# Performance work log

Measured on AMD Instinct MI355X. Metric: run time of the kernel, lower is better.

The kernel has to match this reference:

```python
import jax, jax.numpy as jnp
import numpy as np

B, S, P = 2, 1024, 1024          # batch, new tokens, start_pos (cached prefix)
E, H, KV, HD = 2048, 32, 8, 64    # embed, heads, kv groups, head_dim
G = H // KV                       # group size = 4
THETA = 500000.0
CTX = P + S                       # cache/context length = 2048


def _rope_tables(start, seqlen):
    inv_freq = 1.0 / (THETA ** (jnp.arange(0, HD, 2, dtype=jnp.float32) / HD))
    pos = jnp.arange(start, start + seqlen, dtype=jnp.float32)
    freqs = jnp.outer(pos, inv_freq)              # [S, HD/2]
    emb = jnp.concatenate([freqs, freqs], axis=-1)  # [S, HD]
    return jnp.cos(emb), jnp.sin(emb)


def setup_inputs() -> dict:
    key = jax.random.key(0)
    ks = jax.random.split(key, 8)
    x = jax.random.normal(ks[0], (B, S, E), dtype=jnp.float32)
    cos1, sin1 = _rope_tables(P, S)
    cos = jnp.broadcast_to(cos1[None], (B, S, HD))
    sin = jnp.broadcast_to(sin1[None], (B, S, HD))
    # causal-with-offset additive mask: query i (global pos P+i) sees key j <= P+i
    qpos = P + jnp.arange(S)[:, None]
    kpos = jnp.arange(CTX)[None, :]
    mask = jnp.where(kpos <= qpos, 0.0, -1e9).astype(jnp.float32)[None, None]  # [1,1,S,CTX]
    cache_k = jax.random.normal(ks[1], (B, KV, CTX, HD), dtype=jnp.float32)
    cache_v = jax.random.normal(ks[2], (B, KV, CTX, HD), dtype=jnp.float32)
    sc = 0.02
    Wq = jax.random.normal(ks[3], (E, E), dtype=jnp.float32) * sc
    Wk = jax.random.normal(ks[4], (KV * HD, E), dtype=jnp.float32) * sc
    Wv = jax.random.normal(ks[5], (KV * HD, E), dtype=jnp.float32) * sc
    Wo = jax.random.normal(ks[6], (E, E), dtype=jnp.float32) * sc
    return {"x": x, "cos": cos, "sin": sin, "mask": mask,
            "cache_k": cache_k, "cache_v": cache_v,
            "Wq": Wq, "Wk": Wk, "Wv": Wv, "Wo": Wo, "start_pos": P}


def _rotate_half(t):
    t1, t2 = t[..., : HD // 2], t[..., HD // 2:]
    return jnp.concatenate([-t2, t1], axis=-1)


def _apply_rope(t, cos, sin):
    # t: [B, nh, S, HD]; cos/sin: [B, S, HD] -> unsqueeze head dim
    c = cos[:, None]
    s = sin[:, None]
    return t * c + _rotate_half(t) * s


def reference(x, cos, sin, mask, cache_k, cache_v, Wq, Wk, Wv, Wo, start_pos):
    b, s, e = x.shape
    q = (x @ Wq.T).reshape(b, s, H, HD).transpose(0, 2, 1, 3)    # [B,H,S,HD]
    k = (x @ Wk.T).reshape(b, s, KV, HD).transpose(0, 2, 1, 3)   # [B,KV,S,HD]
    v = (x @ Wv.T).reshape(b, s, KV, HD).transpose(0, 2, 1, 3)
    q = _apply_rope(q, cos, sin)
    k = _apply_rope(k, cos, sin)
    ck = cache_k.at[:, :, start_pos:start_pos + s].set(k)
    cv = cache_v.at[:, :, start_pos:start_pos + s].set(v)
    keys = ck[:, :, : start_pos + s]      # [B,KV,T,HD]
    vals = cv[:, :, : start_pos + s]
    # GQA without materializing repeated KV: view q as [B,KV,G,S,HD]
    qg = q.reshape(b, KV, G, s, HD)
    scores = jnp.einsum("bkgsh,bkth->bkgst", qg, keys) / jnp.sqrt(jnp.float32(HD))
    scores = scores + mask[:, :, None]    # broadcast mask over group dim
    probs = jax.nn.softmax(scores.astype(jnp.float32), axis=-1).astype(x.dtype)
    out = jnp.einsum("bkgst,bkth->bkgsh", probs, vals)            # [B,KV,G,S,HD]
    out = out.reshape(b, H, s, HD).transpose(0, 2, 1, 3).reshape(b, s, e)
    return out @ Wo.T
```

## Files before the change

### kernel.cpp

```cpp
#include <hip/hip_runtime.h>
#include <cstddef>

#define B   2
#define S   1024
#define PP  1024
#define CTX 2048
#define E   2048
#define H   32
#define KVH 8
#define HD  64
#define GQ  4
#define NQKV 3072

typedef short s4v  __attribute__((ext_vector_type(4)));
typedef short s8v  __attribute__((ext_vector_type(8)));
typedef float f4v  __attribute__((ext_vector_type(4)));

__device__ __forceinline__ short f2bf(float f) {
  union { float f; unsigned u; } v; v.f = f;
  unsigned r = v.u + 0x7fffu + ((v.u >> 16) & 1u);
  return (short)(r >> 16);
}
__device__ __forceinline__ float bf2f(short h) {
  union { unsigned u; float f; } v; v.u = ((unsigned)(unsigned short)h) << 16;
  return v.f;
}

__device__ __forceinline__ void gl_lds16(const void* g, void* l) {
  __builtin_amdgcn_global_load_lds((const __attribute__((address_space(1))) unsigned*)g,
                                   (__attribute__((address_space(3))) unsigned*)l, 16, 0, 0);
}

__global__ __launch_bounds__(256) void prep(const float* __restrict__ x,
                                            const float* __restrict__ Wq,
                                            const float* __restrict__ Wk,
                                            const float* __restrict__ Wv,
                                            short* __restrict__ xb,
                                            short* __restrict__ wqkv) {
  const int blk = blockIdx.x, tid = threadIdx.x;
  const float* s; short* d; int base;
  if (blk < 2048)      { s = x;  d = xb;             base = blk; }
  else if (blk < 4096) { s = Wq; d = wqkv;           base = blk - 2048; }
  else if (blk < 4608) { s = Wk; d = wqkv + 4194304; base = blk - 4096; }
  else                 { s = Wv; d = wqkv + 5242880; base = blk - 4608; }
  int i = (base * 256 + tid) * 8;
  float4 a = *(const float4*)&s[i];
  float4 b = *(const float4*)&s[i + 4];
  s8v o;
  o[0]=f2bf(a.x); o[1]=f2bf(a.y); o[2]=f2bf(a.z); o[3]=f2bf(a.w);
  o[4]=f2bf(b.x); o[5]=f2bf(b.y); o[6]=f2bf(b.z); o[7]=f2bf(b.w);
  *(s8v*)&d[i] = o;
}

__global__ __launch_bounds__(256) void qkv_gemm(const short* __restrict__ A,
                                                const short* __restrict__ Bw,
                                                const float* __restrict__ cosb,
                                                const float* __restrict__ sinb,
                                                const float* __restrict__ Wo,
                                                const float* __restrict__ ck,
                                                const float* __restrict__ cv,
                                                short* __restrict__ qb,
                                                short* __restrict__ keys,
                                                short* __restrict__ vt,
                                                short* __restrict__ wob,
                                                float4* __restrict__ outz) {
  __shared__ short As[2][8192];
  __shared__ short Bs[2][8192];
  const int tid = threadIdx.x;
  const int id  = blockIdx.x;

  if (id >= 384) {
    const int aux = id - 384;
    if (aux < 2048) {
      int i = (aux * 256 + tid) * 8;
      float4 a = *(const float4*)&Wo[i];
      float4 b = *(const float4*)&Wo[i + 4];
      s8v o;
      o[0]=f2bf(a.x); o[1]=f2bf(a.y); o[2]=f2bf(a.z); o[3]=f2bf(a.w);
      o[4]=f2bf(b.x); o[5]=f2bf(b.y); o[6]=f2bf(b.z); o[7]=f2bf(b.w);
      *(s8v*)&wob[i] = o;
    } else if (aux < 2560) {
      int idx = (aux - 2048) * 256 + tid;
      int bkv = idx >> 13;
      int rem = idx & 8191;
      size_t off = (size_t)bkv * (CTX * HD) + (size_t)rem * 8;
      float4 a = *(const float4*)&ck[off];
      float4 b = *(const float4*)&ck[off + 4];
      s8v o;
      o[0]=f2bf(a.x); o[1]=f2bf(a.y); o[2]=f2bf(a.z); o[3]=f2bf(a.w);
      o[4]=f2bf(b.x); o[5]=f2bf(b.y); o[6]=f2bf(b.z); o[7]=f2bf(b.w);
      *(s8v*)&keys[off] = o;
    } else if (aux < 2816) {
      short (*Ts)[72] = (short (*)[72])&As[0][0];
      const int blk2 = aux - 2560;
      const int bkv = blk2 >> 4;
      const int p0  = (blk2 & 15) * 64;
      const float* src = cv + (size_t)bkv * CTX * HD + (size_t)p0 * HD;
      {
        int dq = tid & 15, kb = tid >> 4;
        float4 vv[4];
#pragma unroll
        for (int i = 0; i < 4; i++)
          vv[i] = *(const float4*)&src[(size_t)(kb * 4 + i) * HD + dq * 4];
#pragma unroll
        for (int j = 0; j < 4; j++) {
          s4v p;
          p[0]=f2bf(((const float*)&vv[0])[j]); p[1]=f2bf(((const float*)&vv[1])[j]);
          p[2]=f2bf(((const float*)&vv[2])[j]); p[3]=f2bf(((const float*)&vv[3])[j]);
          *(s4v*)&Ts[dq * 4 + j][kb * 4] = p;
        }
      }
      __syncthreads();
      {
        int d = tid >> 2, c = tid & 3;
        short* dst = vt + ((size_t)bkv * HD + d) * CTX + p0 + (c >> 1) * 32 + (c & 1) * 4;
#pragma unroll
        for (int j = 0; j < 4; j++) {
          s4v q4 = *(const s4v*)&Ts[d][c * 16 + j * 4];
          *(s4v*)&dst[j * 8] = q4;
        }
      }
    } else {
      int i0 = (aux - 2816) * 1024 + tid * 4;
#pragma unroll
      for (int j = 0; j < 4; j++) outz[i0 + j] = make_float4(0.f, 0.f, 0.f, 0.f);
    }
    return;
  }

  const int wv   = tid >> 6, lane = tid & 63;
  const int wm   = wv & 1, wn = wv >> 1;
  const int n16  = lane & 15, g = lane >> 4;
  const int m0   = (id / 24) * 128, n0 = (id % 24) * 128;
  const int K = 2048;

  const int rr = tid >> 3;
  const int cc = ((tid & 7) ^ (rr & 7)) * 8;
  const short* pA = A  + (size_t)(m0 + rr) * K + cc;
  const short* pB = Bw + (size_t)(n0 + rr) * K + cc;

  auto stage = [&](int buf, int kofs) {
#pragma unroll
    for (int st = 0; st < 4; st++) {
      gl_lds16(pA + kofs + (size_t)st * 32 * K, &As[buf][(st * 256 + wv * 64) * 8]);
      gl_lds16(pB + kofs + (size_t)st * 32 * K, &Bs[buf][(st * 256 + wv * 64) * 8]);
    }
  };

  f4v acc[4][4] = {};
  stage(0, 0);
  int cur = 0;
  for (int k0 = 0; k0 < K; k0 += 64) {
    __syncthreads();
    if (k0 + 64 < K) stage(cur ^ 1, k0 + 64);

#pragma unroll
    for (int kk = 0; kk < 2; kk++) {
      s8v af[4], bf[4];
#pragma unroll
      for (int mt = 0; mt < 4; mt++)
        af[mt] = *(const s8v*)&As[cur][(wm * 64 + mt * 16 + n16) * 64 + (((kk << 2) | g) ^ (n16 & 7)) * 8];
#pragma unroll
      for (int nt = 0; nt < 4; nt++)
        bf[nt] = *(const s8v*)&Bs[cur][(wn * 64 + nt * 16 + n16) * 64 + (((kk << 2) | g) ^ (n16 & 7)) * 8];
#pragma unroll
      for (int mt = 0; mt < 4; mt++)
#pragma unroll
        for (int nt = 0; nt < 4; nt++)
          acc[mt][nt] = __builtin_amdgcn_mfma_f32_16x16x32_bf16(af[mt], bf[nt], acc[mt][nt], 0, 0, 0);
    }
    cur ^= 1;
  }

  const int rowb = m0 + wm * 64 + g * 4;
  const int colb = n0 + wn * 64 + n16;
  if (n0 < 2048) {
#pragma unroll
    for (int mt = 0; mt < 4; mt++)
#pragma unroll
      for (int nt = 0; nt < 4; nt++) {
        size_t base = (size_t)(rowb + mt * 16) * E + colb + nt * 16;
#pragma unroll
        for (int r = 0; r < 4; r++)
          qb[base + (size_t)r * E] = f2bf(acc[mt][nt][r]);
      }
  } else if (n0 < 2560) {
    const int kvh = ((n0 - 2048) >> 6) + wn;
#pragma unroll
    for (int mt = 0; mt < 4; mt++) {
      const int row = rowb + mt * 16;
      const int bb = row >> 10, s = row & 1023;
      const float* crow = cosb + ((size_t)bb * S + s) * HD;
      const float* srow = sinb + ((size_t)bb * S + s) * HD;
      const size_t kdst = (((size_t)bb * KVH + kvh) * CTX + PP + s) * HD;
#pragma unroll
      for (int nt = 0; nt < 2; nt++) {
        const int d = n16 + nt * 16;
#pragma unroll
        for (int r = 0; r < 4; r++) {
          float c  = crow[r * HD + d];
          float sn = srow[r * HD + d];
          float k1 = acc[mt][nt][r], k2 = acc[mt][nt + 2][r];
          keys[kdst + (size_t)r * HD + d]      = f2bf(k1 * c - k2 * sn);
          keys[kdst + (size_t)r * HD + d + 32] = f2bf(k2 * c + k1 * sn);
        }
      }
    }
  } else {
    const int b    = m0 >> 10;
    const int head = ((n0 - 2560) >> 6) + wn;
    const int sbase = (m0 - (b << 10)) + wm * 64;
    const size_t vrowb = (size_t)(b * KVH + head) * HD;
#pragma unroll
    for (int mt = 0; mt < 4; mt++) {
      const int pos = PP + sbase + ((mt >> 1) << 5) + ((mt & 1) << 2) + (g << 3);
#pragma unroll
      for (int nt = 0; nt < 4; nt++) {
        const int d = nt * 16 + n16;
        s4v o;
        o[0] = f2bf(acc[mt][nt][0]); o[1] = f2bf(acc[mt][nt][1]);
        o[2] = f2bf(acc[mt][nt][2]); o[3] = f2bf(acc[mt][nt][3]);
        *(s4v*)&vt[(vrowb + d) * CTX + pos] = o;
      }
    }
  }
}

__global__ __launch_bounds__(256) void gemm_bf16_sk(const short* __restrict__ A,
                                                    const short* __restrict__ Bw,
                                                    float* __restrict__ C,
                                                    int M, int N, int K) {
  __shared__ short As[2][8192];
  __shared__ short Bs[2][8192];
  const int tid  = threadIdx.x;
  const int wv   = tid >> 6, lane = tid & 63;
  const int wm   = wv & 1, wn = wv >> 1;
  const int n16  = lane & 15, g = lane >> 4;
  const int m0   = blockIdx.y * 128, n0 = blockIdx.x * 128;
  const int kh   = K >> 1;
  const int kbeg = blockIdx.z * kh;

  const int rr = tid >> 3;
  const int cc = ((tid & 7) ^ (rr & 7)) * 8;
  const short* pA = A  + (size_t)(m0 + rr) * K + kbeg + cc;
  const short* pB = Bw + (size_t)(n0 + rr) * K + kbeg + cc;

  auto stage = [&](int buf, int kofs) {
#pragma unroll
    for (int st = 0; st < 4; st++) {
      gl_lds16(pA + kofs + (size_t)st * 32 * K, &As[buf][(st * 256 + wv * 64) * 8]);
      gl_lds16(pB + kofs + (size_t)st * 32 * K, &Bs[buf][(st * 256 + wv * 64) * 8]);
    }
  };

  f4v acc[4][4] = {};
  stage(0, 0);
  int cur = 0;
  for (int k0 = 0; k0 < kh; k0 += 64) {
    __syncthreads();
    if (k0 + 64 < kh) stage(cur ^ 1, k0 + 64);

#pragma unroll
    for (int kk = 0; kk < 2; kk++) {
      s8v af[4], bf[4];
#pragma unroll
      for (int mt = 0; mt < 4; mt++)
        af[mt] = *(const s8v*)&As[cur][(wm * 64 + mt * 16 + n16) * 64 + (((kk << 2) | g) ^ (n16 & 7)) * 8];
#pragma unroll
      for (int nt = 0; nt < 4; nt++)
        bf[nt] = *(const s8v*)&Bs[cur][(wn * 64 + nt * 16 + n16) * 64 + (((kk << 2) | g) ^ (n16 & 7)) * 8];
#pragma unroll
      for (int mt = 0; mt < 4; mt++)
#pragma unroll
        for (int nt = 0; nt < 4; nt++)
          acc[mt][nt] = __builtin_amdgcn_mfma_f32_16x16x32_bf16(af[mt], bf[nt], acc[mt][nt], 0, 0, 0);
    }
    cur ^= 1;
  }

#pragma unroll
  for (int mt = 0; mt < 4; mt++)
#pragma unroll
    for (int nt = 0; nt < 4; nt++) {
      size_t base = (size_t)(m0 + wm * 64 + mt * 16 + g * 4) * N + n0 + wn * 64 + nt * 16 + n16;
#pragma unroll
      for (int r = 0; r < 4; r++)
        unsafeAtomicAdd(&C[base + (size_t)r * N], acc[mt][nt][r]);
    }
}

__global__ __launch_bounds__(256) void attn_mfma(const short* __restrict__ qb,
                                                 const float* __restrict__ cosb,
                                                 const float* __restrict__ sinb,
                                                 const short* __restrict__ keys,
                                                 const short* __restrict__ valsT,
                                                 short* __restrict__ attn) {
  __shared__ short Ks[4096];
  __shared__ short VTs[4096];

  const int xcd  = blockIdx.x & 7;
  const int j    = blockIdx.x >> 3;
  const int sblk = 15 - (j >> 3);
  const int bkv  = xcd * 2 + ((j >> 2) & 1);
  const int b    = bkv >> 3;
  const int kv   = bkv & 7;
  const int h    = kv * 4 + (j & 3);
  const int sq0  = sblk * 64;
  const int kend = PP + sq0 + 64;

  const int tid  = threadIdx.x;
  const int w    = tid >> 6;
  const int lane = tid & 63;
  const int n    = lane & 15;
  const int g    = lane >> 4;

  const short* kbase = keys  + ((size_t)b * KVH + kv) * CTX * HD;
  const short* vtb   = valsT + ((size_t)b * KVH + kv) * (size_t)HD * CTX;

  union { s4v h4[2]; s8v v; } qlo, qhi;
  {
    const size_t row = (size_t)b * S + sq0 + w * 16 + n;
    const short* qrow = qb + row * E + h * 64;
    const float* crow = cosb + row * HD;
    const float* srow = sinb + row * HD;
    const float SC = 0.18033688011112042f;
    s8v q0 = *(const s8v*)&qrow[g * 8];
    s8v q1 = *(const s8v*)&qrow[32 + g * 8];
    float cc[8], ss[8];
    *(float4*)&cc[0] = *(const float4*)&crow[g * 8];
    *(float4*)&cc[4] = *(const float4*)&crow[g * 8 + 4];
    *(float4*)&ss[0] = *(const float4*)&srow[g * 8];
    *(float4*)&ss[4] = *(const float4*)&srow[g * 8 + 4];
#pragma unroll
    for (int j2 = 0; j2 < 8; j2++) {
      float fl = bf2f(q0[j2]), fh = bf2f(q1[j2]);
      qlo.v[j2] = f2bf((fl * cc[j2] - fh * ss[j2]) * SC);
      qhi.v[j2] = f2bf((fh * cc[j2] + fl * ss[j2]) * SC);
    }
  }

  f4v O[4] = {{0,0,0,0},{0,0,0,0},{0,0,0,0},{0,0,0,0}};
  float la[4] = {0.f, 0.f, 0.f, 0.f};
  const int qp     = PP + sq0 + w * 16 + n;
  const int qmin_w = PP + sq0 + w * 16;

  const int lrow = lane >> 3;
  const int sw   = (lane & 7) ^ lrow;
  const short* kg0 = kbase + (size_t)(w * 8 + lrow) * HD + sw * 8;
  const short* kg1 = kg0 + 32 * HD;
  const short* vg0 = vtb + (size_t)(w * 8 + lrow) * CTX + sw * 8;
  const short* vg1 = vg0 + (size_t)32 * CTX;
  short* kl0 = Ks + w * 512;
  short* kl1 = Ks + 2048 + w * 512;
  short* vl0 = VTs + w * 512;
  short* vl1 = VTs + 2048 + w * 512;

  const int xsl = (g ^ (n & 7)) * 8;

  for (int k0 = 0; k0 < kend; k0 += 64) {
    __syncthreads();
    gl_lds16(kg0 + (size_t)k0 * HD, kl0);
    gl_lds16(kg1 + (size_t)k0 * HD, kl1);
    gl_lds16(vg0 + k0, vl0);
    gl_lds16(vg1 + k0, vl1);
    __syncthreads();

    if (k0 >= qmin_w + 16) continue;

    f4v sc[4];
    __builtin_amdgcn_s_setprio(1);
#pragma unroll
    for (int st = 0; st < 4; st++) {
      const short* krow = &Ks[(st * 16 + n) * 64];
      s8v alo = *(const s8v*)(krow + xsl);
      s8v ahi = *(const s8v*)(krow + (xsl ^ 32));
      f4v z = {0.f, 0.f, 0.f, 0.f};
      z = __builtin_amdgcn_mfma_f32_16x16x32_bf16(alo, qlo.v, z, 0, 0, 0);
      sc[st] = __builtin_amdgcn_mfma_f32_16x16x32_bf16(ahi, qhi.v, z, 0, 0, 0);
    }
    __builtin_amdgcn_s_setprio(0);

    if (k0 + 63 > qmin_w) {
#pragma unroll
      for (int st = 0; st < 4; st++)
#pragma unroll
        for (int r = 0; r < 4; r++) {
          int kpos = k0 + st * 16 + g * 4 + r;
          if (kpos > qp) sc[st][r] = -3e38f;
        }
    }

    union { unsigned u[4]; s8v v; } pb0, pb1;
#pragma unroll
    for (int st = 0; st < 4; st++) {
      float e0 = __builtin_amdgcn_exp2f(sc[st][0]);
      float e1 = __builtin_amdgcn_exp2f(sc[st][1]);
      float e2 = __builtin_amdgcn_exp2f(sc[st][2]);
      float e3 = __builtin_amdgcn_exp2f(sc[st][3]);
      la[0] += e0; la[1] += e1; la[2] += e2; la[3] += e3;
      unsigned w0, w1;
      asm("v_cvt_pk_bf16_f32 %0, %1, %2" : "=v"(w0) : "v"(e0), "v"(e1));
      asm("v_cvt_pk_bf16_f32 %0, %1, %2" : "=v"(w1) : "v"(e2), "v"(e3));
      if (st < 2) { pb0.u[st * 2] = w0; pb0.u[st * 2 + 1] = w1; }
      else        { pb1.u[(st - 2) * 2] = w0; pb1.u[(st - 2) * 2 + 1] = w1; }
    }

    __builtin_amdgcn_s_setprio(1);
#pragma unroll
    for (int dg = 0; dg < 4; dg++) {
      const short* vr = &VTs[(dg * 16 + n) * 64];
      s8v va = *(const s8v*)(vr + xsl);
      s8v vx = *(const s8v*)(vr + (xsl ^ 32));
      O[dg] = __builtin_amdgcn_mfma_f32_16x16x32_bf16(va, pb0.v, O[dg], 0, 0, 0);
      O[dg] = __builtin_amdgcn_mfma_f32_16x16x32_bf16(vx, pb1.v, O[dg], 0, 0, 0);
    }
    __builtin_amdgcn_s_setprio(0);
  }

  float l = (la[0] + la[1]) + (la[2] + la[3]);
  l += __shfl_xor(l, 16);
  l += __shfl_xor(l, 32);
  const float rl = 1.f / l;
  short* orow = attn + ((size_t)b * S + sq0 + w * 16 + n) * E + h * 64;
#pragma unroll
  for (int dg = 0; dg < 4; dg++) {
    s4v o;
    o[0] = f2bf(O[dg][0] * rl); o[1] = f2bf(O[dg][1] * rl);
    o[2] = f2bf(O[dg][2] * rl); o[3] = f2bf(O[dg][3] * rl);
    *(s4v*)&orow[dg * 16 + g * 4] = o;
  }
}

extern "C" void kernel_launch(void* const* d_in, const int* in_sizes, int n_in,
                              void* d_out, int out_size, void* d_ws, size_t ws_size,
                              hipStream_t stream) {
  const float* x       = (const float*)d_in[0];
  const float* cosb    = (const float*)d_in[1];
  const float* sinb    = (const float*)d_in[2];
  const float* cache_k = (const float*)d_in[4];
  const float* cache_v = (const float*)d_in[5];
  const float* Wq      = (const float*)d_in[6];
  const float* Wk      = (const float*)d_in[7];
  const float* Wv      = (const float*)d_in[8];
  const float* Wo      = (const float*)d_in[9];
  float* out = (float*)d_out;

  short* xb    = (short*)d_ws;
  short* wqkv  = xb + 4194304;
  short* wob   = wqkv + 6291456;
  short* keysb = wob + 4194304;
  short* valsT = keysb + 2097152;
  short* aout  = valsT + 2097152;
  short* qb    = aout + 4194304;

  dim3 blk(256);

  prep<<<5120, blk, 0, stream>>>(x, Wq, Wk, Wv, xb, wqkv);

  qkv_gemm<<<4224, blk, 0, stream>>>(xb, wqkv, cosb, sinb, Wo, cache_k, cache_v,
                                     qb, keysb, valsT, wob, (float4*)out);

  attn_mfma<<<B * H * (S / 64), blk, 0, stream>>>(qb, cosb, sinb, keysb, valsT, aout);

  gemm_bf16_sk<<<dim3(E / 128, (B * S) / 128, 2), blk, 0, stream>>>(aout, wob, out, B * S, E, E);
}
```

Before: 243.4 us.

## Shrink GEMM tiles to 128x64 and replace split-K atomics with direct stores

Both the QKV projection and the output projection now use 128x64 tiles, with each of the four waves owning 32 rows across the full 64 columns. This doubles the block count to fill more CUs. The output projection drops its two-way split-K with float atomics and its zero-fill pass in favour of one block per tile that writes results directly. The trade-off is lower arithmetic intensity per block (more global and LDS traffic per MFMA) and a longer K loop per block in the output projection.

```diff
diff --git a/kernel.cpp b/kernel.cpp
--- a/kernel.cpp
+++ b/kernel.cpp
@@ -62,15 +62,14 @@
                                                 short* __restrict__ qb,
                                                 short* __restrict__ keys,
                                                 short* __restrict__ vt,
-                                                short* __restrict__ wob,
-                                                float4* __restrict__ outz) {
+                                                short* __restrict__ wob) {
   __shared__ short As[2][8192];
-  __shared__ short Bs[2][8192];
+  __shared__ short Bs[2][4096];
   const int tid = threadIdx.x;
   const int id  = blockIdx.x;
 
-  if (id >= 384) {
-    const int aux = id - 384;
+  if (id >= 768) {
+    const int aux = id - 768;
     if (aux < 2048) {
       int i = (aux * 256 + tid) * 8;
       float4 a = *(const float4*)&Wo[i];
@@ -90,7 +89,7 @@
       o[0]=f2bf(a.x); o[1]=f2bf(a.y); o[2]=f2bf(a.z); o[3]=f2bf(a.w);
       o[4]=f2bf(b.x); o[5]=f2bf(b.y); o[6]=f2bf(b.z); o[7]=f2bf(b.w);
       *(s8v*)&keys[off] = o;
-    } else if (aux < 2816) {
+    } else {
       short (*Ts)[72] = (short (*)[72])&As[0][0];
       const int blk2 = aux - 2560;
       const int bkv = blk2 >> 4;
@@ -120,18 +119,13 @@
           *(s4v*)&dst[j * 8] = q4;
         }
       }
-    } else {
-      int i0 = (aux - 2816) * 1024 + tid * 4;
-#pragma unroll
-      for (int j = 0; j < 4; j++) outz[i0 + j] = make_float4(0.f, 0.f, 0.f, 0.f);
     }
     return;
   }
 
   const int wv   = tid >> 6, lane = tid & 63;
-  const int wm   = wv & 1, wn = wv >> 1;
   const int n16  = lane & 15, g = lane >> 4;
-  const int m0   = (id / 24) * 128, n0 = (id % 24) * 128;
+  const int m0   = (id / 48) * 128, n0 = (id % 48) * 64;
   const int K = 2048;
 
   const int rr = tid >> 3;
@@ -141,13 +135,14 @@
 
   auto stage = [&](int buf, int kofs) {
 #pragma unroll
-    for (int st = 0; st < 4; st++) {
+    for (int st = 0; st < 4; st++)
       gl_lds16(pA + kofs + (size_t)st * 32 * K, &As[buf][(st * 256 + wv * 64) * 8]);
+#pragma unroll
+    for (int st = 0; st < 2; st++)
       gl_lds16(pB + kofs + (size_t)st * 32 * K, &Bs[buf][(st * 256 + wv * 64) * 8]);
-    }
   };
 
-  f4v acc[4][4] = {};
+  f4v acc[2][4] = {};
   stage(0, 0);
   int cur = 0;
   for (int k0 = 0; k0 < K; k0 += 64) {
@@ -156,15 +151,16 @@
 
 #pragma unroll
     for (int kk = 0; kk < 2; kk++) {
-      s8v af[4], bf[4];
-#pragma unroll
-      for (int mt = 0; mt < 4; mt++)
-        af[mt] = *(const s8v*)&As[cur][(wm * 64 + mt * 16 + n16) * 64 + (((kk << 2) | g) ^ (n16 & 7)) * 8];
+      const int slot = (((kk << 2) | g) ^ (n16 & 7)) * 8;
+      s8v af[2], bf[4];
+#pragma unroll
+      for (int mt = 0; mt < 2; mt++)
+        af[mt] = *(const s8v*)&As[cur][(wv * 32 + mt * 16 + n16) * 64 + slot];
 #pragma unroll
       for (int nt = 0; nt < 4; nt++)
-        bf[nt] = *(const s8v*)&Bs[cur][(wn * 64 + nt * 16 + n16) * 64 + (((kk << 2) | g) ^ (n16 & 7)) * 8];
-#pragma unroll
-      for (int mt = 0; mt < 4; mt++)
+        bf[nt] = *(const s8v*)&Bs[cur][(nt * 16 + n16) * 64 + slot];
+#pragma unroll
+      for (int mt = 0; mt < 2; mt++)
 #pragma unroll
         for (int nt = 0; nt < 4; nt++)
           acc[mt][nt] = __builtin_amdgcn_mfma_f32_16x16x32_bf16(af[mt], bf[nt], acc[mt][nt], 0, 0, 0);
@@ -172,22 +168,21 @@
     cur ^= 1;
   }
 
-  const int rowb = m0 + wm * 64 + g * 4;
-  const int colb = n0 + wn * 64 + n16;
+  const int rowb = m0 + wv * 32 + g * 4;
   if (n0 < 2048) {
 #pragma unroll
-    for (int mt = 0; mt < 4; mt++)
+    for (int mt = 0; mt < 2; mt++)
 #pragma unroll
       for (int nt = 0; nt < 4; nt++) {
-        size_t base = (size_t)(rowb + mt * 16) * E + colb + nt * 16;
+        size_t base = (size_t)(rowb + mt * 16) * E + n0 + nt * 16 + n16;
 #pragma unroll
         for (int r = 0; r < 4; r++)
           qb[base + (size_t)r * E] = f2bf(acc[mt][nt][r]);
       }
   } else if (n0 < 2560) {
-    const int kvh = ((n0 - 2048) >> 6) + wn;
-#pragma unroll
-    for (int mt = 0; mt < 4; mt++) {
+    const int kvh = (n0 - 2048) >> 6;
+#pragma unroll
+    for (int mt = 0; mt < 2; mt++) {
       const int row = rowb + mt * 16;
       const int bb = row >> 10, s = row & 1023;
       const float* crow = cosb + ((size_t)bb * S + s) * HD;
@@ -208,12 +203,13 @@
     }
   } else {
     const int b    = m0 >> 10;
-    const int head = ((n0 - 2560) >> 6) + wn;
-    const int sbase = (m0 - (b << 10)) + wm * 64;
+    const int head = (n0 - 2560) >> 6;
+    const int sbase = (m0 - (b << 10)) + (wv >> 1) * 64;
     const size_t vrowb = (size_t)(b * KVH + head) * HD;
 #pragma unroll
-    for (int mt = 0; mt < 4; mt++) {
-      const int pos = PP + sbase + ((mt >> 1) << 5) + ((mt & 1) << 2) + (g << 3);
+    for (int mt = 0; mt < 2; mt++) {
+      const int mtp = (wv & 1) * 2 + mt;
+      const int pos = PP + sbase + ((mtp >> 1) << 5) + ((mtp & 1) << 2) + (g << 3);
 #pragma unroll
       for (int nt = 0; nt < 4; nt++) {
         const int d = nt * 16 + n16;
@@ -226,51 +222,51 @@
   }
 }
 
-__global__ __launch_bounds__(256) void gemm_bf16_sk(const short* __restrict__ A,
-                                                    const short* __restrict__ Bw,
-                                                    float* __restrict__ C,
-                                                    int M, int N, int K) {
+__global__ __launch_bounds__(256) void oproj_gemm(const short* __restrict__ A,
+                                                  const short* __restrict__ Bw,
+                                                  float* __restrict__ C) {
   __shared__ short As[2][8192];
-  __shared__ short Bs[2][8192];
+  __shared__ short Bs[2][4096];
   const int tid  = threadIdx.x;
   const int wv   = tid >> 6, lane = tid & 63;
-  const int wm   = wv & 1, wn = wv >> 1;
   const int n16  = lane & 15, g = lane >> 4;
-  const int m0   = blockIdx.y * 128, n0 = blockIdx.x * 128;
-  const int kh   = K >> 1;
-  const int kbeg = blockIdx.z * kh;
+  const int id   = blockIdx.x;
+  const int m0   = (id >> 5) * 128, n0 = (id & 31) * 64;
+  const int K = E, N = E;
 
   const int rr = tid >> 3;
   const int cc = ((tid & 7) ^ (rr & 7)) * 8;
-  const short* pA = A  + (size_t)(m0 + rr) * K + kbeg + cc;
-  const short* pB = Bw + (size_t)(n0 + rr) * K + kbeg + cc;
+  const short* pA = A  + (size_t)(m0 + rr) * K + cc;
+  const short* pB = Bw + (size_t)(n0 + rr) * K + cc;
 
   auto stage = [&](int buf, int kofs) {
 #pragma unroll
-    for (int st = 0; st < 4; st++) {
+    for (int st = 0; st < 4; st++)
       gl_lds16(pA + kofs + (size_t)st * 32 * K, &As[buf][(st * 256 + wv * 64) * 8]);
+#pragma unroll
+    for (int st = 0; st < 2; st++)
       gl_lds16(pB + kofs + (size_t)st * 32 * K, &Bs[buf][(st * 256 + wv * 64) * 8]);
-    }
   };
 
-  f4v acc[4][4] = {};
+  f4v acc[2][4] = {};
   stage(0, 0);
   int cur = 0;
-  for (int k0 = 0; k0 < kh; k0 += 64) {
+  for (int k0 = 0; k0 < K; k0 += 64) {
     __syncthreads();
-    if (k0 + 64 < kh) stage(cur ^ 1, k0 + 64);
+    if (k0 + 64 < K) stage(cur ^ 1, k0 + 64);
 
 #pragma unroll
     for (int kk = 0; kk < 2; kk++) {
-      s8v af[4], bf[4];
-#pragma unroll
-      for (int mt = 0; mt < 4; mt++)
-        af[mt] = *(const s8v*)&As[cur][(wm * 64 + mt * 16 + n16) * 64 + (((kk << 2) | g) ^ (n16 & 7)) * 8];
+      const int slot = (((kk << 2) | g) ^ (n16 & 7)) * 8;
+      s8v af[2], bf[4];
+#pragma unroll
+      for (int mt = 0; mt < 2; mt++)
+        af[mt] = *(const s8v*)&As[cur][(wv * 32 + mt * 16 + n16) * 64 + slot];
 #pragma unroll
       for (int nt = 0; nt < 4; nt++)
-        bf[nt] = *(const s8v*)&Bs[cur][(wn * 64 + nt * 16 + n16) * 64 + (((kk << 2) | g) ^ (n16 & 7)) * 8];
-#pragma unroll
-      for (int mt = 0; mt < 4; mt++)
+        bf[nt] = *(const s8v*)&Bs[cur][(nt * 16 + n16) * 64 + slot];
+#pragma unroll
+      for (int mt = 0; mt < 2; mt++)
 #pragma unroll
         for (int nt = 0; nt < 4; nt++)
           acc[mt][nt] = __builtin_amdgcn_mfma_f32_16x16x32_bf16(af[mt], bf[nt], acc[mt][nt], 0, 0, 0);
@@ -279,13 +275,13 @@
   }
 
 #pragma unroll
-  for (int mt = 0; mt < 4; mt++)
+  for (int mt = 0; mt < 2; mt++)
 #pragma unroll
     for (int nt = 0; nt < 4; nt++) {
-      size_t base = (size_t)(m0 + wm * 64 + mt * 16 + g * 4) * N + n0 + wn * 64 + nt * 16 + n16;
+      size_t base = (size_t)(m0 + wv * 32 + mt * 16 + g * 4) * N + n0 + nt * 16 + n16;
 #pragma unroll
       for (int r = 0; r < 4; r++)
-        unsafeAtomicAdd(&C[base + (size_t)r * N], acc[mt][nt][r]);
+        C[base + (size_t)r * N] = acc[mt][nt][r];
     }
 }
 
@@ -457,10 +453,10 @@
 
   prep<<<5120, blk, 0, stream>>>(x, Wq, Wk, Wv, xb, wqkv);
 
-  qkv_gemm<<<4224, blk, 0, stream>>>(xb, wqkv, cosb, sinb, Wo, cache_k, cache_v,
-                                     qb, keysb, valsT, wob, (float4*)out);
+  qkv_gemm<<<3584, blk, 0, stream>>>(xb, wqkv, cosb, sinb, Wo, cache_k, cache_v,
+                                     qb, keysb, valsT, wob);
 
   attn_mfma<<<B * H * (S / 64), blk, 0, stream>>>(qb, cosb, sinb, keysb, valsT, aout);
 
-  gemm_bf16_sk<<<dim3(E / 128, (B * S) / 128, 2), blk, 0, stream>>>(aout, wob, out, B * S, E, E);
-}
+  oproj_gemm<<<512, blk, 0, stream>>>(aout, wob, out);
+}
```

Result: faster. 229.4 us (-5.8%).
